# Kernel tuning notes

Hardware: AMD Instinct MI355X
Metric: run time of the kernel (lower is better)

## Reference

```python
import jax, jax.numpy as jnp
import numpy as np

# Config (matches init_kwargs)
N_PARTS = 4
N_DATASETS = 2
N_VOLUMES = 16
N_TRANSFORMS = 2
TEMP_FAC = 0.1
BS = N_PARTS * N_DATASETS * N_VOLUMES          # 128
N_TOTAL = BS * (N_TRANSFORMS + 1)              # 384 rows in reg_pred
D_FEAT = 131072
PD = N_PARTS * N_DATASETS                      # class period for denominator exclusion
EPS = 1e-6


def setup_inputs() -> dict:
    key = jax.random.key(0)
    reg_pred = jax.random.normal(key, (N_TOTAL, D_FEAT), dtype=jnp.float32)
    return {"reg_pred": reg_pred}


def reference(reg_pred) -> jnp.ndarray:
    # Cosine similarity with torch's eps clamp on each norm.
    norms = jnp.maximum(jnp.linalg.norm(reg_pred, axis=1, keepdims=True), EPS)
    xn = reg_pred / norms                                   # [N, D]
    sims = (xn @ xn.T) / TEMP_FAC                           # [N, N] full cos-sim matrix
    e = jnp.exp(sims)

    # Denominator for pos_index p excludes every column j with j % PD == p % PD
    # (dataset_similar=False, within_dataset=False). Precompute per-class column sums.
    jmod = jnp.arange(N_TOTAL) % PD                          # [N]
    class_sum = jax.ops.segment_sum(e.T, jmod, num_segments=PD).T  # [N, PD]
    row_sum = jnp.sum(e, axis=1)                             # [N]

    p = jnp.arange(BS)
    rem = p % PD
    i1 = p
    i2 = BS + p
    i3 = (p + PD) % N_TOTAL
    i4 = (BS + p + PD) % N_TOTAL
    i5 = 2 * BS + p
    i6 = (2 * BS + p + PD) % N_TOTAL

    def pair_loss(a, b):
        en = e[a, b]                                         # exp(cos(xi,xj)/t), [BS]
        den_a = row_sum[a] - class_sum[a, rem]               # sum exp over den indexes
        den_b = row_sum[b] - class_sum[b, rem]
        return jnp.sum(-jnp.log(en / (en + den_a)) - jnp.log(en / (en + den_b)))

    total = (pair_loss(i1, i2) + pair_loss(i3, i4) + pair_loss(i1, i3)
             + pair_loss(i2, i4) + pair_loss(i5, i6) + pair_loss(i2, i5)
             + pair_loss(i4, i6))
    return total / (N_TRANSFORMS * 3 * BS)
```

## Files before the change

### kernel.cpp

```cpp
#include <hip/hip_runtime.h>
#include <hip/hip_bf16.h>

#define N_TOTAL 384
#define BS 128
#define PD 8
#define D_FEAT 131072
#define EPS 1e-6f

#define NSTRIP 128
#define COLS_PER (D_FEAT / NSTRIP)
#define CHUNK 32
#define NCH (COLS_PER / CHUNK)
#define LROW 64
#define NSLOT 12
#define PSTRIDE (NSLOT * 4096)

typedef __attribute__((ext_vector_type(4))) float f32x4;
typedef __attribute__((ext_vector_type(8))) __bf16 bf16x8;
typedef __attribute__((ext_vector_type(4))) __bf16 bf16x4;

static __device__ const int RBt[16]  = {0,1,2,3,4,4,5,5,  0,1,0,1,2,2,3,3};
static __device__ const int CB0t[16] = {0,0,2,2,4,5,4,5,  2,2,4,4,4,5,4,5};
static __device__ const int CB1t[16] = {1,1,3,3,-1,-1,-1,-1,  3,3,5,5,-1,-1,-1,-1};

__device__ __forceinline__ float gsym(const float* __restrict__ G, int i, int j) {
    return ((i >> 7) <= (j >> 7)) ? G[(size_t)i * N_TOTAL + j]
                                  : G[(size_t)j * N_TOTAL + i];
}

__global__ __launch_bounds__(512, 2) void gram_fused_kernel(const float* __restrict__ X,
                                                            float* __restrict__ P) {
    __shared__ char sm[2][N_TOTAL * LROW];

    const int B      = blockIdx.x;
    const int x      = B & 7;
    const int i      = B >> 3;
    const int flavor = i & 1;
    const int strip  = x + 8 * (i >> 1);

    const int tid  = threadIdx.x;
    const int wave = tid >> 6;
    const int lane = tid & 63;
    const int r16  = lane & 15;
    const int kg   = lane >> 4;

    const int rb   = RBt[flavor * 8 + wave] * 64;
    const int cb0  = CB0t[flavor * 8 + wave] * 64;
    const int cb1s = CB1t[flavor * 8 + wave];
    const int cb1  = cb1s * 64;
    const int rdoff = (kg * 16) ^ ((r16 & 7) << 4);

    const size_t cbase = (size_t)strip * COLS_PER;
    const int srow  = tid >> 3;
    const int scolf = (tid & 7) * 4;
    const int wbase = srow * LROW + (((tid & 7) * 8) ^ ((srow & 7) << 4));

    f32x4 acc0[4][4], acc1[4][4];
#pragma unroll
    for (int m = 0; m < 4; m++)
#pragma unroll
        for (int n = 0; n < 4; n++) { acc0[m][n] = (f32x4)(0.0f); acc1[m][n] = (f32x4)(0.0f); }

    float4 g[6];

#define LOADG(t)                                                                          \
    _Pragma("unroll") for (int s = 0; s < 6; s++)                                         \
        g[s] = *(const float4*)(X + (size_t)(srow + s * 64) * D_FEAT + cbase +            \
                                (size_t)(t) * CHUNK + scolf);

#define WRITEL(buf)                                                                       \
    _Pragma("unroll") for (int s = 0; s < 6; s++) {                                       \
        bf16x4 v;                                                                         \
        v[0] = (__bf16)g[s].x; v[1] = (__bf16)g[s].y;                                     \
        v[2] = (__bf16)g[s].z; v[3] = (__bf16)g[s].w;                                     \
        *(bf16x4*)(&sm[buf][wbase + s * 64 * LROW]) = v;                                  \
    }

#define COMPUTE(buf)                                                                      \
    do {                                                                                  \
        const char* bptr = sm[buf];                                                       \
        bf16x8 af[4], bf0[4];                                                             \
        _Pragma("unroll") for (int m = 0; m < 4; m++)                                     \
            af[m] = *(const bf16x8*)(bptr + (rb + m * 16 + r16) * LROW + rdoff);          \
        _Pragma("unroll") for (int n = 0; n < 4; n++)                                     \
            bf0[n] = *(const bf16x8*)(bptr + (cb0 + n * 16 + r16) * LROW + rdoff);        \
        _Pragma("unroll") for (int m = 0; m < 4; m++)                                     \
            _Pragma("unroll") for (int n = 0; n < 4; n++)                                 \
                acc0[m][n] = __builtin_amdgcn_mfma_f32_16x16x32_bf16(af[m], bf0[n],       \
                                                                     acc0[m][n], 0, 0, 0);\
        if (cb1s >= 0) {                                                                  \
            bf16x8 bf1[4];                                                                \
            _Pragma("unroll") for (int n = 0; n < 4; n++)                                 \
                bf1[n] = *(const bf16x8*)(bptr + (cb1 + n * 16 + r16) * LROW + rdoff);    \
            _Pragma("unroll") for (int m = 0; m < 4; m++)                                 \
                _Pragma("unroll") for (int n = 0; n < 4; n++)                             \
                    acc1[m][n] = __builtin_amdgcn_mfma_f32_16x16x32_bf16(af[m], bf1[n],   \
                                                                     acc1[m][n], 0, 0, 0);\
        }                                                                                 \
    } while (0)

    LOADG(0);
    WRITEL(0);
    LOADG(1);
    __syncthreads();

    for (int t = 0; t < NCH; ++t) {
        const int cur = t & 1;
        COMPUTE(cur);
        if (t + 1 < NCH) {
            WRITEL(cur ^ 1);
            if (t + 2 < NCH) LOADG(t + 2);
        }
        __syncthreads();
    }
#undef LOADG
#undef WRITEL
#undef COMPUTE

    const int crow = (lane >> 4) * 4;
    const int ccol = lane & 15;
    float* base0 = P + ((size_t)(strip * 2 + flavor) * NSLOT + wave) * 4096;
#pragma unroll
    for (int m = 0; m < 4; m++)
#pragma unroll
        for (int n = 0; n < 4; n++)
            *(f32x4*)(base0 + (n * 16 + ccol) * 64 + m * 16 + crow) = acc0[m][n];
    if (cb1s >= 0) {
        float* base1 = P + ((size_t)(strip * 2 + flavor) * NSLOT + 8 + wave) * 4096;
#pragma unroll
        for (int m = 0; m < 4; m++)
#pragma unroll
            for (int n = 0; n < 4; n++)
                *(f32x4*)(base1 + (n * 16 + ccol) * 64 + m * 16 + crow) = acc1[m][n];
    }
}

__global__ __launch_bounds__(256) void reduce_kernel(const float* __restrict__ P,
                                                     float* __restrict__ G) {
    const int b     = blockIdx.x;
    const int chunk = b & 15;
    const int sg    = b >> 4;
    const int f     = sg / NSLOT;
    const int slot  = sg % NSLOT;
    const int e     = chunk * 256 + threadIdx.x;

    const float* p = P + ((size_t)f * NSLOT + slot) * 4096 + e;
    float s = 0.0f;
#pragma unroll 8
    for (int strip = 0; strip < NSTRIP; ++strip)
        s += p[(size_t)strip * 2 * PSTRIDE];

    const int w     = (slot < 8) ? slot : slot - 8;
    const int rb    = RBt[f * 8 + w] * 64;
    const int cb    = ((slot < 8) ? CB0t[f * 8 + w] : CB1t[f * 8 + w]) * 64;
    const int col   = e >> 6;
    const int row   = e & 63;
    G[(size_t)(rb + row) * N_TOTAL + cb + col] = s;
}

__global__ __launch_bounds__(128) void den_kernel(const float* __restrict__ G,
                                                  float* __restrict__ den) {
    const int i = blockIdx.x;
    __shared__ float sInv[N_TOTAL];
    for (int j = threadIdx.x; j < N_TOTAL; j += 128) {
        const float n = sqrtf(G[(size_t)j * N_TOTAL + j]);
        sInv[j] = 1.0f / fmaxf(n, EPS);
    }
    __syncthreads();

    const float mi  = sInv[i] * 10.0f;
    const int   myc = i & 7;
    float s = 0.0f;
    for (int j = threadIdx.x; j < N_TOTAL; j += 128) {
        if ((j & 7) != myc)
            s += expf(gsym(G, i, j) * mi * sInv[j]);
    }
#pragma unroll
    for (int off = 32; off > 0; off >>= 1) s += __shfl_down(s, off, 64);
    __shared__ float partial[2];
    if ((threadIdx.x & 63) == 0) partial[threadIdx.x >> 6] = s;
    __syncthreads();
    if (threadIdx.x == 0) den[i] = partial[0] + partial[1];
}

__global__ __launch_bounds__(256) void loss_kernel(const float* __restrict__ G,
                                                   const float* __restrict__ den,
                                                   float* __restrict__ out) {
    __shared__ float sInv[N_TOTAL];
    for (int j = threadIdx.x; j < N_TOTAL; j += 256) {
        const float n = sqrtf(G[(size_t)j * N_TOTAL + j]);
        sInv[j] = 1.0f / fmaxf(n, EPS);
    }
    __syncthreads();

    float s = 0.0f;
    for (int idx = threadIdx.x; idx < 7 * BS; idx += 256) {
        const int p   = idx & (BS - 1);
        const int set = idx >> 7;
        int a, b;
        switch (set) {
            case 0:  a = p;                        b = BS + p;                      break;
            case 1:  a = (p + PD) % N_TOTAL;       b = (BS + p + PD) % N_TOTAL;     break;
            case 2:  a = p;                        b = (p + PD) % N_TOTAL;          break;
            case 3:  a = BS + p;                   b = (BS + p + PD) % N_TOTAL;     break;
            case 4:  a = 2 * BS + p;               b = (2 * BS + p + PD) % N_TOTAL; break;
            case 5:  a = BS + p;                   b = 2 * BS + p;                  break;
            default: a = (BS + p + PD) % N_TOTAL;  b = (2 * BS + p + PD) % N_TOTAL; break;
        }
        const float en = expf(gsym(G, a, b) * sInv[a] * sInv[b] * 10.0f);
        s += log1pf(den[a] / en) + log1pf(den[b] / en);
    }
#pragma unroll
    for (int off = 32; off > 0; off >>= 1) s += __shfl_down(s, off, 64);
    __shared__ float partial[4];
    if ((threadIdx.x & 63) == 0) partial[threadIdx.x >> 6] = s;
    __syncthreads();
    if (threadIdx.x == 0)
        out[0] = (partial[0] + partial[1] + partial[2] + partial[3]) / 768.0f;
}

extern "C" void kernel_launch(void* const* d_in, const int* in_sizes, int n_in,
                              void* d_out, int out_size, void* d_ws, size_t ws_size,
                              hipStream_t stream) {
    (void)in_sizes; (void)n_in; (void)out_size; (void)ws_size;
    const float* X   = (const float*)d_in[0];
    float*       out = (float*)d_out;
    float*       G   = (float*)d_ws;
    float*       den = G + (size_t)N_TOTAL * N_TOTAL;
    float*       P   = (float*)((char*)d_ws + (1u << 20));

    gram_fused_kernel<<<NSTRIP * 2, 512, 0, stream>>>(X, P);
    reduce_kernel<<<384, 256, 0, stream>>>(P, G);
    den_kernel<<<N_TOTAL, 128, 0, stream>>>(G, den);
    loss_kernel<<<1, 256, 0, stream>>>(G, den, out);
}
```

Baseline: 77.78 us.

## Compute all 21 Gram tiles per strip in one block with bf16 partials

Each block now handles a whole feature strip and computes all upper-triangle 64x64 tiles, three per wave, instead of splitting the tiles across two flavour blocks that each reload the same strip. This halves global reads of X. The strip count doubles to 256, and the per-strip partial sums are stored as bf16 to cut partial-buffer traffic. The costs are higher register pressure from three accumulator sets (the occupancy hint of 2 was dropped) and lower precision in the partial sums before reduction.

```diff
diff --git a/kernel.cpp b/kernel.cpp
--- a/kernel.cpp
+++ b/kernel.cpp
@@ -7,47 +7,43 @@
 #define D_FEAT 131072
 #define EPS 1e-6f
 
-#define NSTRIP 128
+#define NSTRIP 256
 #define COLS_PER (D_FEAT / NSTRIP)
 #define CHUNK 32
 #define NCH (COLS_PER / CHUNK)
 #define LROW 64
-#define NSLOT 12
-#define PSTRIDE (NSLOT * 4096)
+#define NSLOT 24
 
 typedef __attribute__((ext_vector_type(4))) float f32x4;
 typedef __attribute__((ext_vector_type(8))) __bf16 bf16x8;
 typedef __attribute__((ext_vector_type(4))) __bf16 bf16x4;
 
-static __device__ const int RBt[16]  = {0,1,2,3,4,4,5,5,  0,1,0,1,2,2,3,3};
-static __device__ const int CB0t[16] = {0,0,2,2,4,5,4,5,  2,2,4,4,4,5,4,5};
-static __device__ const int CB1t[16] = {1,1,3,3,-1,-1,-1,-1,  3,3,5,5,-1,-1,-1,-1};
+static __device__ const int SUBA[8][3] = {
+    {0,0,2},{1,1,2},{2,2,3},{3,3,3},{4,0,0},{4,1,1},{5,0,0},{5,1,1}};
+static __device__ const int SUBB[8][3] = {
+    {0,1,4},{0,1,5},{2,3,4},{2,3,5},{4,2,3},{5,2,3},{4,4,5},{5,4,5}};
+static __device__ const int SRB[NSLOT] = {0,0,2, 1,1,2, 2,2,3, 3,3,3, 4,0,0, 4,1,1, 5,0,0, 5,1,1};
+static __device__ const int SCB[NSLOT] = {0,1,4, 0,1,5, 2,3,4, 2,3,5, 4,2,3, 5,2,3, 4,4,5, 5,4,5};
 
 __device__ __forceinline__ float gsym(const float* __restrict__ G, int i, int j) {
     return ((i >> 7) <= (j >> 7)) ? G[(size_t)i * N_TOTAL + j]
                                   : G[(size_t)j * N_TOTAL + i];
 }
 
-__global__ __launch_bounds__(512, 2) void gram_fused_kernel(const float* __restrict__ X,
-                                                            float* __restrict__ P) {
+__global__ __launch_bounds__(512) void gram_fused_kernel(const float* __restrict__ X,
+                                                         __bf16* __restrict__ P) {
     __shared__ char sm[2][N_TOTAL * LROW];
 
-    const int B      = blockIdx.x;
-    const int x      = B & 7;
-    const int i      = B >> 3;
-    const int flavor = i & 1;
-    const int strip  = x + 8 * (i >> 1);
-
+    const int strip = blockIdx.x;
     const int tid  = threadIdx.x;
     const int wave = tid >> 6;
     const int lane = tid & 63;
     const int r16  = lane & 15;
     const int kg   = lane >> 4;
 
-    const int rb   = RBt[flavor * 8 + wave] * 64;
-    const int cb0  = CB0t[flavor * 8 + wave] * 64;
-    const int cb1s = CB1t[flavor * 8 + wave];
-    const int cb1  = cb1s * 64;
+    const int a0 = SUBA[wave][0] * 64, b0 = SUBB[wave][0] * 64;
+    const int a1 = SUBA[wave][1] * 64, b1 = SUBB[wave][1] * 64;
+    const int a2 = SUBA[wave][2] * 64, b2 = SUBB[wave][2] * 64;
     const int rdoff = (kg * 16) ^ ((r16 & 7) << 4);
 
     const size_t cbase = (size_t)strip * COLS_PER;
@@ -55,11 +51,13 @@
     const int scolf = (tid & 7) * 4;
     const int wbase = srow * LROW + (((tid & 7) * 8) ^ ((srow & 7) << 4));
 
-    f32x4 acc0[4][4], acc1[4][4];
+    f32x4 acc0[4][4], acc1[4][4], acc2[4][4];
 #pragma unroll
     for (int m = 0; m < 4; m++)
 #pragma unroll
-        for (int n = 0; n < 4; n++) { acc0[m][n] = (f32x4)(0.0f); acc1[m][n] = (f32x4)(0.0f); }
+        for (int n = 0; n < 4; n++) {
+            acc0[m][n] = (f32x4)(0.0f); acc1[m][n] = (f32x4)(0.0f); acc2[m][n] = (f32x4)(0.0f);
+        }
 
     float4 g[6];
 
@@ -76,27 +74,25 @@
         *(bf16x4*)(&sm[buf][wbase + s * 64 * LROW]) = v;                                  \
     }
 
+#define SUBT(accX, ab, bb)                                                                \
+    do {                                                                                  \
+        bf16x8 af[4], bf[4];                                                              \
+        _Pragma("unroll") for (int m = 0; m < 4; m++)                                     \
+            af[m] = *(const bf16x8*)(bptr + (ab + m * 16 + r16) * LROW + rdoff);          \
+        _Pragma("unroll") for (int n = 0; n < 4; n++)                                     \
+            bf[n] = *(const bf16x8*)(bptr + (bb + n * 16 + r16) * LROW + rdoff);          \
+        _Pragma("unroll") for (int m = 0; m < 4; m++)                                     \
+            _Pragma("unroll") for (int n = 0; n < 4; n++)                                 \
+                accX[m][n] = __builtin_amdgcn_mfma_f32_16x16x32_bf16(af[m], bf[n],        \
+                                                                     accX[m][n], 0, 0, 0);\
+    } while (0)
+
 #define COMPUTE(buf)                                                                      \
     do {                                                                                  \
         const char* bptr = sm[buf];                                                       \
-        bf16x8 af[4], bf0[4];                                                             \
-        _Pragma("unroll") for (int m = 0; m < 4; m++)                                     \
-            af[m] = *(const bf16x8*)(bptr + (rb + m * 16 + r16) * LROW + rdoff);          \
-        _Pragma("unroll") for (int n = 0; n < 4; n++)                                     \
-            bf0[n] = *(const bf16x8*)(bptr + (cb0 + n * 16 + r16) * LROW + rdoff);        \
-        _Pragma("unroll") for (int m = 0; m < 4; m++)                                     \
-            _Pragma("unroll") for (int n = 0; n < 4; n++)                                 \
-                acc0[m][n] = __builtin_amdgcn_mfma_f32_16x16x32_bf16(af[m], bf0[n],       \
-                                                                     acc0[m][n], 0, 0, 0);\
-        if (cb1s >= 0) {                                                                  \
-            bf16x8 bf1[4];                                                                \
-            _Pragma("unroll") for (int n = 0; n < 4; n++)                                 \
-                bf1[n] = *(const bf16x8*)(bptr + (cb1 + n * 16 + r16) * LROW + rdoff);    \
-            _Pragma("unroll") for (int m = 0; m < 4; m++)                                 \
-                _Pragma("unroll") for (int n = 0; n < 4; n++)                             \
-                    acc1[m][n] = __builtin_amdgcn_mfma_f32_16x16x32_bf16(af[m], bf1[n],   \
-                                                                     acc1[m][n], 0, 0, 0);\
-        }                                                                                 \
+        SUBT(acc0, a0, b0);                                                               \
+        SUBT(acc1, a1, b1);                                                               \
+        SUBT(acc2, a2, b2);                                                               \
     } while (0)
 
     LOADG(0);
@@ -115,46 +111,45 @@
     }
 #undef LOADG
 #undef WRITEL
+#undef SUBT
 #undef COMPUTE
 
     const int crow = (lane >> 4) * 4;
     const int ccol = lane & 15;
-    float* base0 = P + ((size_t)(strip * 2 + flavor) * NSLOT + wave) * 4096;
-#pragma unroll
-    for (int m = 0; m < 4; m++)
-#pragma unroll
-        for (int n = 0; n < 4; n++)
-            *(f32x4*)(base0 + (n * 16 + ccol) * 64 + m * 16 + crow) = acc0[m][n];
-    if (cb1s >= 0) {
-        float* base1 = P + ((size_t)(strip * 2 + flavor) * NSLOT + 8 + wave) * 4096;
-#pragma unroll
-        for (int m = 0; m < 4; m++)
-#pragma unroll
-            for (int n = 0; n < 4; n++)
-                *(f32x4*)(base1 + (n * 16 + ccol) * 64 + m * 16 + crow) = acc1[m][n];
-    }
-}
-
-__global__ __launch_bounds__(256) void reduce_kernel(const float* __restrict__ P,
+#define STOREP(accX, s)                                                                   \
+    do {                                                                                  \
+        __bf16* base = P + ((size_t)strip * NSLOT + wave * 3 + (s)) * 4096;               \
+        _Pragma("unroll") for (int m = 0; m < 4; m++)                                     \
+            _Pragma("unroll") for (int n = 0; n < 4; n++) {                               \
+                bf16x4 v;                                                                 \
+                v[0] = (__bf16)accX[m][n][0]; v[1] = (__bf16)accX[m][n][1];               \
+                v[2] = (__bf16)accX[m][n][2]; v[3] = (__bf16)accX[m][n][3];               \
+                *(bf16x4*)(base + (n * 16 + ccol) * 64 + m * 16 + crow) = v;              \
+            }                                                                             \
+    } while (0)
+    STOREP(acc0, 0);
+    STOREP(acc1, 1);
+    STOREP(acc2, 2);
+#undef STOREP
+}
+
+__global__ __launch_bounds__(256) void reduce_kernel(const __bf16* __restrict__ P,
                                                      float* __restrict__ G) {
     const int b     = blockIdx.x;
     const int chunk = b & 15;
-    const int sg    = b >> 4;
-    const int f     = sg / NSLOT;
-    const int slot  = sg % NSLOT;
+    const int slot  = b >> 4;
     const int e     = chunk * 256 + threadIdx.x;
 
-    const float* p = P + ((size_t)f * NSLOT + slot) * 4096 + e;
+    const __bf16* p = P + (size_t)slot * 4096 + e;
     float s = 0.0f;
-#pragma unroll 8
+#pragma unroll 16
     for (int strip = 0; strip < NSTRIP; ++strip)
-        s += p[(size_t)strip * 2 * PSTRIDE];
-
-    const int w     = (slot < 8) ? slot : slot - 8;
-    const int rb    = RBt[f * 8 + w] * 64;
-    const int cb    = ((slot < 8) ? CB0t[f * 8 + w] : CB1t[f * 8 + w]) * 64;
-    const int col   = e >> 6;
-    const int row   = e & 63;
+        s += (float)p[(size_t)strip * NSLOT * 4096];
+
+    const int rb  = SRB[slot] * 64;
+    const int cb  = SCB[slot] * 64;
+    const int col = e >> 6;
+    const int row = e & 63;
     G[(size_t)(rb + row) * N_TOTAL + cb + col] = s;
 }
 
@@ -227,10 +222,10 @@
     float*       out = (float*)d_out;
     float*       G   = (float*)d_ws;
     float*       den = G + (size_t)N_TOTAL * N_TOTAL;
-    float*       P   = (float*)((char*)d_ws + (1u << 20));
-
-    gram_fused_kernel<<<NSTRIP * 2, 512, 0, stream>>>(X, P);
-    reduce_kernel<<<384, 256, 0, stream>>>(P, G);
+    __bf16*      P   = (__bf16*)((char*)d_ws + (1u << 20));
+
+    gram_fused_kernel<<<NSTRIP, 512, 0, stream>>>(X, P);
+    reduce_kernel<<<NSLOT * 16, 256, 0, stream>>>(P, G);
     den_kernel<<<N_TOTAL, 128, 0, stream>>>(G, den);
     loss_kernel<<<1, 256, 0, stream>>>(G, den, out);
 }
```

After: 89.56 us. 1.15x slower.
